# Performance work log

Measured on AMD Instinct MI355X. Metric: run time of the kernel, lower is better.

Reference implementation:

```python
import jax, jax.numpy as jnp
import numpy as np

BN_EPS = 1e-5


def setup_inputs() -> dict:
    key = jax.random.key(0)
    ks = jax.random.split(key, 8)
    N, Cin, Cout, D, H, W = 4, 512, 256, 256, 128, 128
    feat_ffm = jax.random.normal(ks[0], (N, Cin, H, W), dtype=jnp.float32)
    coarse_x = jax.random.normal(ks[1], (N, D, H, W), dtype=jnp.float32)
    # conv1: 1x1, no bias; BN (eval mode: running stats); conv2: 1x1 with bias
    w1 = jax.random.normal(ks[2], (Cout, Cin), dtype=jnp.float32) * (1.0 / np.sqrt(Cin))
    bn_gamma = jnp.ones((Cout,), dtype=jnp.float32)
    bn_beta = jnp.zeros((Cout,), dtype=jnp.float32)
    bn_mean = jax.random.normal(ks[3], (Cout,), dtype=jnp.float32) * 0.1
    bn_var = jax.random.uniform(ks[4], (Cout,), dtype=jnp.float32, minval=0.5, maxval=1.5)
    w2 = jax.random.normal(ks[5], (Cout, Cout), dtype=jnp.float32) * (1.0 / np.sqrt(Cout))
    b2 = jnp.zeros((Cout,), dtype=jnp.float32)
    return {"feat_ffm": feat_ffm, "coarse_x": coarse_x, "w1": w1,
            "bn_gamma": bn_gamma, "bn_beta": bn_beta, "bn_mean": bn_mean,
            "bn_var": bn_var, "w2": w2, "b2": b2}


def reference(feat_ffm, coarse_x, w1, bn_gamma, bn_beta, bn_mean, bn_var, w2, b2):
    N, D, H, W = coarse_x.shape
    # conv1 (1x1) + BN(eval) + ReLU; Dropout2d is identity in eval mode
    x = jnp.einsum('nihw,oi->nohw', feat_ffm, w1)
    scale = bn_gamma * jax.lax.rsqrt(bn_var + BN_EPS)
    x = x * scale[None, :, None, None] + (bn_beta - bn_mean * scale)[None, :, None, None]
    x = jax.nn.relu(x)  # [N, C, H, W]
    C = x.shape[1]
    q = coarse_x.reshape(N, D, H * W)          # proj_query / proj_value
    k = x.reshape(N, C, H * W)                 # proj_key (pre-permute)
    energy = jnp.einsum('nds,ncs->ndc', q, k)  # [N, D, C]
    energy_new = jnp.max(energy, axis=-1, keepdims=True) - energy
    attention = jax.nn.softmax(energy_new, axis=-1)        # [N, D, C]
    out = jnp.einsum('ndc,nds->ncs', attention, q)         # attention^T @ value
    out = out.reshape(N, C, H, W)
    out = jnp.einsum('nchw,oc->nohw', out, w2) + b2[None, :, None, None]
    return out
```

## Files before the change

kernel.cpp:

```cpp
#include <hip/hip_runtime.h>


#define S_DIM 16384
#define C_DIM 256
#define CIN 512

typedef unsigned short u16;
typedef _Float16 f16;
typedef __attribute__((ext_vector_type(8))) _Float16 f16x8;
typedef __attribute__((ext_vector_type(4))) float f32x4;

__device__ __forceinline__ u16 f2h(float x) {
    f16 h = (f16)x;
    return *(u16*)&h;
}
__device__ __forceinline__ float h2f(u16 u) {
    f16 h = *(f16*)&u;
    return (float)h;
}
__device__ __forceinline__ void gld16(const u16* g, u16* l) {
    __builtin_amdgcn_global_load_lds((const __attribute__((address_space(1))) void*)g,
                                     (__attribute__((address_space(3))) void*)l, 16, 0, 0);
}
__device__ __forceinline__ void gld16f(const float* g, float* l) {
    __builtin_amdgcn_global_load_lds((const __attribute__((address_space(1))) void*)g,
                                     (__attribute__((address_space(3))) void*)l, 16, 0, 0);
}

__global__ __launch_bounds__(256) void prep_kernel(
    const float* __restrict__ coarse, const float* __restrict__ w1,
    const float* __restrict__ gamma, const float* __restrict__ beta,
    const float* __restrict__ mean, const float* __restrict__ var,
    u16* __restrict__ qhi, u16* __restrict__ qlo,
    u16* __restrict__ w1hi, u16* __restrict__ w1lo, float* __restrict__ b1) {
    int b = blockIdx.x;
    int t = threadIdx.x;
    if (b < 4096) {
        size_t i = (size_t)b * 256 + t;
        for (size_t c = i; c < 4194304u; c += 1048576u) {
            float4 v = ((const float4*)coarse)[c];
            float vv[4] = {v.x, v.y, v.z, v.w};
            u16 h[4], l[4];
#pragma unroll
            for (int j = 0; j < 4; ++j) {
                h[j] = f2h(vv[j]);
                l[j] = f2h(vv[j] - h2f(h[j]));
            }
            *(uint2*)&qhi[c * 4] = *(uint2*)h;
            *(uint2*)&qlo[c * 4] = *(uint2*)l;
        }
    } else {
        int o = (b - 4096) * 16 + (t >> 4);
        int lane16 = t & 15;
        float sc = gamma[o] * rsqrtf(var[o] + 1e-5f);
        for (int i = lane16; i < CIN; i += 16) {
            float v = w1[o * CIN + i] * sc;
            u16 h = f2h(v);
            w1hi[o * CIN + i] = h;
            w1lo[o * CIN + i] = f2h(v - h2f(h));
        }
        if (lane16 == 0) b1[o] = beta[o] - mean[o] * sc;
    }
}

__global__ __launch_bounds__(256) void conv_kernel(
    const u16* __restrict__ w1hi, const u16* __restrict__ w1lo,
    const float* __restrict__ feat, const float* __restrict__ b1,
    u16* __restrict__ khi, u16* __restrict__ klo) {
    __shared__ u16 AhS[4096], AlS[4096];
    __shared__ float BfS[4096];
    int s0 = blockIdx.x * 128;
    int m0 = blockIdx.y * 128;
    int bz = blockIdx.z;
    int tid = threadIdx.x, wave = tid >> 6, lane = tid & 63;
    int quad = lane >> 4, l15 = lane & 15;
    int wm = wave >> 1, wn = wave & 1;

    int Lr = lane >> 2, Ls = lane & 3;
    int koff = (Ls ^ ((Lr >> 1) & 3)) * 8;
    const u16* gAh = w1hi + (size_t)(m0 + wave * 32 + Lr) * CIN + koff;
    const u16* gAl = w1lo + (size_t)(m0 + wave * 32 + Lr) * CIN + koff;
    u16* dAh = AhS + wave * 1024;
    u16* dAl = AlS + wave * 1024;

    int bcol = ((lane & 31) * 4) ^ ((wave & 1) << 4);
    const float* gB = feat + (size_t)bz * ((size_t)CIN * S_DIM)
                    + (size_t)(8 * wave + (lane >> 5)) * S_DIM + s0 + bcol;
    float* dB = BfS + wave * 1024;

    f32x4 zero = {0.f, 0.f, 0.f, 0.f};
    f32x4 acc[4][4];
#pragma unroll
    for (int i = 0; i < 4; ++i)
#pragma unroll
        for (int j = 0; j < 4; ++j) acc[i][j] = zero;

    for (int kb = 0; kb < CIN; kb += 32) {
        __syncthreads();
        gld16(gAh + kb, dAh);
        gld16(gAh + kb + 16 * CIN, dAh + 512);
        gld16(gAl + kb, dAl);
        gld16(gAl + kb + 16 * CIN, dAl + 512);
#pragma unroll
        for (int p = 0; p < 4; ++p)
            gld16f(gB + (size_t)(kb + 2 * p) * S_DIM, dB + p * 256);
        __syncthreads();

        f16x8 a_h[4], a_l[4];
        int axor = ((l15 >> 1) & 3);
        int ao = (wm * 64 + l15) * 32 + ((quad ^ axor) * 8);
#pragma unroll
        for (int t = 0; t < 4; ++t) {
            a_h[t] = *(const f16x8*)&AhS[ao + t * 512];
            a_l[t] = *(const f16x8*)&AlS[ao + t * 512];
        }
        f16x8 b_s[4];
        int fl = (quad & 1) << 4;
        const float* Brow = BfS + quad * 1024;
#pragma unroll
        for (int nt = 0; nt < 4; ++nt) {
            int nf = (wn * 64 + nt * 16 + l15) ^ fl;
            union { u16 u[8]; f16x8 v; } T;
#pragma unroll
            for (int j = 0; j < 8; ++j) T.u[j] = f2h(Brow[j * 128 + nf]);
            b_s[nt] = T.v;
        }
#pragma unroll
        for (int mt = 0; mt < 4; ++mt)
#pragma unroll
            for (int nt = 0; nt < 4; ++nt) {
                acc[mt][nt] = __builtin_amdgcn_mfma_f32_16x16x32_f16(a_h[mt], b_s[nt], acc[mt][nt], 0, 0, 0);
                acc[mt][nt] = __builtin_amdgcn_mfma_f32_16x16x32_f16(a_l[mt], b_s[nt], acc[mt][nt], 0, 0, 0);
            }
    }

#pragma unroll
    for (int mt = 0; mt < 4; ++mt) {
#pragma unroll
        for (int r = 0; r < 4; ++r) {
            int row = m0 + wm * 64 + mt * 16 + quad * 4 + r;
            float bi = b1[row];
#pragma unroll
            for (int nt = 0; nt < 4; ++nt) {
                int cc = s0 + wn * 64 + nt * 16 + l15;
                float v = fmaxf(acc[mt][nt][r] + bi, 0.f);
                u16 h = f2h(v);
                size_t o = (size_t)bz * 4194304 + (size_t)row * S_DIM + cc;
                khi[o] = h;
                klo[o] = f2h(v - h2f(h));
            }
        }
    }
}

__global__ __launch_bounds__(256) void energy_kernel(
    const u16* __restrict__ qhi, const u16* __restrict__ qlo,
    const u16* __restrict__ khi, const u16* __restrict__ klo,
    float* __restrict__ Ep) {
    __shared__ u16 AhS[4096], BhS[4096], AlS[4096], BlS[4096];
    int kBeg = blockIdx.x * 512;
    int m0 = (blockIdx.y >> 1) * 128;
    int n0 = (blockIdx.y & 1) * 128;
    int bz = blockIdx.z;
    int tid = threadIdx.x, wave = tid >> 6, lane = tid & 63;
    int quad = lane >> 4, l15 = lane & 15;
    int wm = wave >> 1, wn = wave & 1;

    int Lr = lane >> 2, Ls = lane & 3;
    int koff = (Ls ^ ((Lr >> 1) & 3)) * 8;
    size_t bo = (size_t)bz * 4194304;
    const u16* gAh = qhi + bo + (size_t)(m0 + wave * 32 + Lr) * S_DIM + kBeg + koff;
    const u16* gAl = qlo + bo + (size_t)(m0 + wave * 32 + Lr) * S_DIM + kBeg + koff;
    const u16* gBh = khi + bo + (size_t)(n0 + wave * 32 + Lr) * S_DIM + kBeg + koff;
    const u16* gBl = klo + bo + (size_t)(n0 + wave * 32 + Lr) * S_DIM + kBeg + koff;
    u16* dAh = AhS + wave * 1024;
    u16* dAl = AlS + wave * 1024;
    u16* dBh = BhS + wave * 1024;
    u16* dBl = BlS + wave * 1024;

    f32x4 zero = {0.f, 0.f, 0.f, 0.f};
    f32x4 acc[4][4];
#pragma unroll
    for (int i = 0; i < 4; ++i)
#pragma unroll
        for (int j = 0; j < 4; ++j) acc[i][j] = zero;

    const size_t row16 = (size_t)16 * S_DIM;
    for (int kb = 0; kb < 512; kb += 32) {
        __syncthreads();
        gld16(gAh + kb, dAh);
        gld16(gAh + kb + row16, dAh + 512);
        gld16(gBh + kb, dBh);
        gld16(gBh + kb + row16, dBh + 512);
        gld16(gAl + kb, dAl);
        gld16(gAl + kb + row16, dAl + 512);
        gld16(gBl + kb, dBl);
        gld16(gBl + kb + row16, dBl + 512);
        __syncthreads();

        f16x8 a_h[4], b_h[4], a_l[4], b_l[4];
        int axor = ((l15 >> 1) & 3);
        int aOff = (wm * 64 + l15) * 32 + ((quad ^ axor) * 8);
        int bOff = (wn * 64 + l15) * 32 + ((quad ^ axor) * 8);
#pragma unroll
        for (int t = 0; t < 4; ++t) {
            a_h[t] = *(const f16x8*)&AhS[aOff + t * 512];
            b_h[t] = *(const f16x8*)&BhS[bOff + t * 512];
            a_l[t] = *(const f16x8*)&AlS[aOff + t * 512];
            b_l[t] = *(const f16x8*)&BlS[bOff + t * 512];
        }
#pragma unroll
        for (int mt = 0; mt < 4; ++mt)
#pragma unroll
            for (int nt = 0; nt < 4; ++nt) {
                acc[mt][nt] = __builtin_amdgcn_mfma_f32_16x16x32_f16(a_h[mt], b_h[nt], acc[mt][nt], 0, 0, 0);
                acc[mt][nt] = __builtin_amdgcn_mfma_f32_16x16x32_f16(a_h[mt], b_l[nt], acc[mt][nt], 0, 0, 0);
                acc[mt][nt] = __builtin_amdgcn_mfma_f32_16x16x32_f16(a_l[mt], b_h[nt], acc[mt][nt], 0, 0, 0);
            }
    }

    float* Ce = Ep + ((size_t)(blockIdx.x * 4 + bz)) * 65536;
#pragma unroll
    for (int mt = 0; mt < 4; ++mt)
#pragma unroll
        for (int r = 0; r < 4; ++r) {
            int row = m0 + wm * 64 + mt * 16 + quad * 4 + r;
#pragma unroll
            for (int nt = 0; nt < 4; ++nt) {
                int cc = n0 + wn * 64 + nt * 16 + l15;
                Ce[(size_t)row * C_DIM + cc] = acc[mt][nt][r];
            }
        }
}

__global__ __launch_bounds__(256) void softmax_kernel(const float* __restrict__ Ep,
                                                      float* __restrict__ att) {
    __shared__ float red[4], red2[4];
    int b = blockIdx.x;
    int t = threadIdx.x;
    const float* p = Ep + (size_t)b * 256 + t;
    float v = 0.f;
#pragma unroll 8
    for (int s = 0; s < 32; ++s) v += p[(size_t)s * 262144];
    float m = v;
#pragma unroll
    for (int o = 32; o > 0; o >>= 1) m = fminf(m, __shfl_xor(m, o, 64));
    int lane = t & 63, wid = t >> 6;
    if (lane == 0) red[wid] = m;
    __syncthreads();
    m = fminf(fminf(red[0], red[1]), fminf(red[2], red[3]));
    float e = expf(m - v);
    float s = e;
#pragma unroll
    for (int o = 32; o > 0; o >>= 1) s += __shfl_xor(s, o, 64);
    if (lane == 0) red2[wid] = s;
    __syncthreads();
    s = red2[0] + red2[1] + red2[2] + red2[3];
    att[(size_t)b * 256 + t] = e / s;
}

__global__ __launch_bounds__(256) void m2h_kernel(const float* __restrict__ w2,
                                                  const float* __restrict__ att,
                                                  u16* __restrict__ M2h) {
    int t = blockIdx.x * 256 + threadIdx.x;
    int d = t & 255, o = (t >> 8) & 255, n = t >> 16;
    const float4* wr = (const float4*)(w2 + (size_t)o * C_DIM);
    const float4* ar = (const float4*)(att + ((size_t)n * C_DIM + d) * C_DIM);
    float s = 0.0f;
#pragma unroll 4
    for (int c4 = 0; c4 < 64; ++c4) {
        float4 w = wr[c4];
        float4 a = ar[c4];
        s += w.x * a.x + w.y * a.y + w.z * a.z + w.w * a.w;
    }
    M2h[((size_t)n * C_DIM + o) * C_DIM + d] = f2h(s);
}

__global__ __launch_bounds__(256) void final_kernel(
    const u16* __restrict__ M2h, const float* __restrict__ coarse,
    const float* __restrict__ b2, float* __restrict__ out) {
    __shared__ u16 AhS[4096];
    __shared__ float BfS[4096];
    int s0 = blockIdx.x * 128;
    int m0 = blockIdx.y * 128;
    int bz = blockIdx.z;
    int tid = threadIdx.x, wave = tid >> 6, lane = tid & 63;
    int quad = lane >> 4, l15 = lane & 15;
    int wm = wave >> 1, wn = wave & 1;

    int Lr = lane >> 2, Ls = lane & 3;
    int koff = (Ls ^ ((Lr >> 1) & 3)) * 8;
    const u16* gA = M2h + (size_t)bz * 65536 + (size_t)(m0 + wave * 32 + Lr) * C_DIM + koff;
    u16* dA = AhS + wave * 1024;
    int bcol = ((lane & 31) * 4) ^ ((wave & 1) << 4);
    const float* gB = coarse + (size_t)bz * 4194304
                    + (size_t)(8 * wave + (lane >> 5)) * S_DIM + s0 + bcol;
    float* dB = BfS + wave * 1024;

    f32x4 zero = {0.f, 0.f, 0.f, 0.f};
    f32x4 acc[4][4];
#pragma unroll
    for (int i = 0; i < 4; ++i)
#pragma unroll
        for (int j = 0; j < 4; ++j) acc[i][j] = zero;

    for (int kb = 0; kb < C_DIM; kb += 32) {
        __syncthreads();
        gld16(gA + kb, dA);
        gld16(gA + kb + 16 * C_DIM, dA + 512);
#pragma unroll
        for (int p = 0; p < 4; ++p)
            gld16f(gB + (size_t)(kb + 2 * p) * S_DIM, dB + p * 256);
        __syncthreads();

        f16x8 a_s[4];
        int axor = ((l15 >> 1) & 3);
        int ao = (wm * 64 + l15) * 32 + ((quad ^ axor) * 8);
#pragma unroll
        for (int t = 0; t < 4; ++t) a_s[t] = *(const f16x8*)&AhS[ao + t * 512];
        f16x8 b_s[4];
        int fl = (quad & 1) << 4;
        const float* Brow = BfS + quad * 1024;
#pragma unroll
        for (int nt = 0; nt < 4; ++nt) {
            int nf = (wn * 64 + nt * 16 + l15) ^ fl;
            union { u16 u[8]; f16x8 v; } T;
#pragma unroll
            for (int j = 0; j < 8; ++j) T.u[j] = f2h(Brow[j * 128 + nf]);
            b_s[nt] = T.v;
        }
#pragma unroll
        for (int mt = 0; mt < 4; ++mt)
#pragma unroll
            for (int nt = 0; nt < 4; ++nt)
                acc[mt][nt] = __builtin_amdgcn_mfma_f32_16x16x32_f16(a_s[mt], b_s[nt], acc[mt][nt], 0, 0, 0);
    }

#pragma unroll
    for (int mt = 0; mt < 4; ++mt)
#pragma unroll
        for (int r = 0; r < 4; ++r) {
            int row = m0 + wm * 64 + mt * 16 + quad * 4 + r;
            float bi = b2[row];
#pragma unroll
            for (int nt = 0; nt < 4; ++nt) {
                int cc = s0 + wn * 64 + nt * 16 + l15;
                out[(size_t)bz * 4194304 + (size_t)row * S_DIM + cc] = acc[mt][nt][r] + bi;
            }
        }
}

extern "C" void kernel_launch(void* const* d_in, const int* in_sizes, int n_in,
                              void* d_out, int out_size, void* d_ws, size_t ws_size,
                              hipStream_t stream) {
    const float* feat   = (const float*)d_in[0];
    const float* coarse = (const float*)d_in[1];
    const float* w1     = (const float*)d_in[2];
    const float* gamma  = (const float*)d_in[3];
    const float* beta   = (const float*)d_in[4];
    const float* mean   = (const float*)d_in[5];
    const float* var    = (const float*)d_in[6];
    const float* w2     = (const float*)d_in[7];
    const float* b2     = (const float*)d_in[8];
    float* out = (float*)d_out;

    char* base = (char*)d_ws;
    u16* qhi   = (u16*)(base);
    u16* qlo   = (u16*)(base + 33554432);
    u16* khi   = (u16*)(base + 67108864);
    u16* klo   = (u16*)(base + 100663296);
    float* Ep  = (float*)(base + 134217728);
    float* att = (float*)(base + 201326592);
    u16* M2h   = (u16*)(base + 202375168);
    u16* w1hi  = (u16*)(base + 202899456);
    u16* w1lo  = (u16*)(base + 203161600);
    float* b1  = (float*)(base + 203423744);

    prep_kernel<<<4112, 256, 0, stream>>>(coarse, w1, gamma, beta, mean, var,
                                          qhi, qlo, w1hi, w1lo, b1);

    conv_kernel<<<dim3(128, 2, 4), 256, 0, stream>>>(w1hi, w1lo, feat, b1, khi, klo);

    energy_kernel<<<dim3(32, 4, 4), 256, 0, stream>>>(qhi, qlo, khi, klo, Ep);

    softmax_kernel<<<1024, 256, 0, stream>>>(Ep, att);

    m2h_kernel<<<1024, 256, 0, stream>>>(w2, att, M2h);

    final_kernel<<<dim3(128, 2, 4), 256, 0, stream>>>(M2h, coarse, b2, out);
}
```

Measured before the change: 428.6 us.

## Double-buffer LDS tiles in conv, energy and final GEMM kernels

The conv, energy and final GEMM kernels now keep two LDS buffers per operand. Each iteration issues the async global-to-LDS loads for the next K tile before computing on the current one, leaving one barrier per iteration instead of two. The aim is to hide global load latency behind the MFMA work. In exchange, LDS use per block doubles, which can lower occupancy, and the compiler may still insert conservative waits that remove the overlap.

Result: no change. 423.1 us (-1.3%).

```diff
diff --git a/kernel.cpp b/kernel.cpp
--- a/kernel.cpp
+++ b/kernel.cpp
@@ -25,6 +25,17 @@
 __device__ __forceinline__ void gld16f(const float* g, float* l) {
     __builtin_amdgcn_global_load_lds((const __attribute__((address_space(1))) void*)g,
                                      (__attribute__((address_space(3))) void*)l, 16, 0, 0);
+}
+
+__device__ __forceinline__ void stage_pair(const u16* g, int kb, size_t row16,
+                                           u16* d, int wave) {
+    gld16(g + kb, d + wave * 1024);
+    gld16(g + kb + row16, d + wave * 1024 + 512);
+}
+__device__ __forceinline__ void stage_b(const float* g, int kb, float* d, int wave) {
+#pragma unroll
+    for (int p = 0; p < 4; ++p)
+        gld16f(g + (size_t)(kb + 2 * p) * S_DIM, d + wave * 1024 + p * 256);
 }
 
 __global__ __launch_bounds__(256) void prep_kernel(
@@ -67,8 +78,8 @@
     const u16* __restrict__ w1hi, const u16* __restrict__ w1lo,
     const float* __restrict__ feat, const float* __restrict__ b1,
     u16* __restrict__ khi, u16* __restrict__ klo) {
-    __shared__ u16 AhS[4096], AlS[4096];
-    __shared__ float BfS[4096];
+    __shared__ u16 AhS[2][4096], AlS[2][4096];
+    __shared__ float BfS[2][4096];
     int s0 = blockIdx.x * 128;
     int m0 = blockIdx.y * 128;
     int bz = blockIdx.z;
@@ -80,13 +91,9 @@
     int koff = (Ls ^ ((Lr >> 1) & 3)) * 8;
     const u16* gAh = w1hi + (size_t)(m0 + wave * 32 + Lr) * CIN + koff;
     const u16* gAl = w1lo + (size_t)(m0 + wave * 32 + Lr) * CIN + koff;
-    u16* dAh = AhS + wave * 1024;
-    u16* dAl = AlS + wave * 1024;
-
     int bcol = ((lane & 31) * 4) ^ ((wave & 1) << 4);
     const float* gB = feat + (size_t)bz * ((size_t)CIN * S_DIM)
                     + (size_t)(8 * wave + (lane >> 5)) * S_DIM + s0 + bcol;
-    float* dB = BfS + wave * 1024;
 
     f32x4 zero = {0.f, 0.f, 0.f, 0.f};
     f32x4 acc[4][4];
@@ -95,28 +102,30 @@
 #pragma unroll
         for (int j = 0; j < 4; ++j) acc[i][j] = zero;
 
+    stage_pair(gAh, 0, 16 * CIN, AhS[0], wave);
+    stage_pair(gAl, 0, 16 * CIN, AlS[0], wave);
+    stage_b(gB, 0, BfS[0], wave);
+    __syncthreads();
+
+    int cur = 0;
     for (int kb = 0; kb < CIN; kb += 32) {
-        __syncthreads();
-        gld16(gAh + kb, dAh);
-        gld16(gAh + kb + 16 * CIN, dAh + 512);
-        gld16(gAl + kb, dAl);
-        gld16(gAl + kb + 16 * CIN, dAl + 512);
-#pragma unroll
-        for (int p = 0; p < 4; ++p)
-            gld16f(gB + (size_t)(kb + 2 * p) * S_DIM, dB + p * 256);
-        __syncthreads();
+        if (kb + 32 < CIN) {
+            stage_pair(gAh, kb + 32, 16 * CIN, AhS[cur ^ 1], wave);
+            stage_pair(gAl, kb + 32, 16 * CIN, AlS[cur ^ 1], wave);
+            stage_b(gB, kb + 32, BfS[cur ^ 1], wave);
+        }
 
         f16x8 a_h[4], a_l[4];
         int axor = ((l15 >> 1) & 3);
         int ao = (wm * 64 + l15) * 32 + ((quad ^ axor) * 8);
 #pragma unroll
         for (int t = 0; t < 4; ++t) {
-            a_h[t] = *(const f16x8*)&AhS[ao + t * 512];
-            a_l[t] = *(const f16x8*)&AlS[ao + t * 512];
+            a_h[t] = *(const f16x8*)&AhS[cur][ao + t * 512];
+            a_l[t] = *(const f16x8*)&AlS[cur][ao + t * 512];
         }
         f16x8 b_s[4];
         int fl = (quad & 1) << 4;
-        const float* Brow = BfS + quad * 1024;
+        const float* Brow = BfS[cur] + quad * 1024;
 #pragma unroll
         for (int nt = 0; nt < 4; ++nt) {
             int nf = (wn * 64 + nt * 16 + l15) ^ fl;
@@ -132,6 +141,8 @@
                 acc[mt][nt] = __builtin_amdgcn_mfma_f32_16x16x32_f16(a_h[mt], b_s[nt], acc[mt][nt], 0, 0, 0);
                 acc[mt][nt] = __builtin_amdgcn_mfma_f32_16x16x32_f16(a_l[mt], b_s[nt], acc[mt][nt], 0, 0, 0);
             }
+        __syncthreads();
+        cur ^= 1;
     }
 
 #pragma unroll
@@ -157,7 +168,7 @@
     const u16* __restrict__ qhi, const u16* __restrict__ qlo,
     const u16* __restrict__ khi, const u16* __restrict__ klo,
     float* __restrict__ Ep) {
-    __shared__ u16 AhS[4096], BhS[4096], AlS[4096], BlS[4096];
+    __shared__ u16 AhS[2][4096], BhS[2][4096], AlS[2][4096], BlS[2][4096];
     int kBeg = blockIdx.x * 512;
     int m0 = (blockIdx.y >> 1) * 128;
     int n0 = (blockIdx.y & 1) * 128;
@@ -173,10 +184,6 @@
     const u16* gAl = qlo + bo + (size_t)(m0 + wave * 32 + Lr) * S_DIM + kBeg + koff;
     const u16* gBh = khi + bo + (size_t)(n0 + wave * 32 + Lr) * S_DIM + kBeg + koff;
     const u16* gBl = klo + bo + (size_t)(n0 + wave * 32 + Lr) * S_DIM + kBeg + koff;
-    u16* dAh = AhS + wave * 1024;
-    u16* dAl = AlS + wave * 1024;
-    u16* dBh = BhS + wave * 1024;
-    u16* dBl = BlS + wave * 1024;
 
     f32x4 zero = {0.f, 0.f, 0.f, 0.f};
     f32x4 acc[4][4];
@@ -186,17 +193,20 @@
         for (int j = 0; j < 4; ++j) acc[i][j] = zero;
 
     const size_t row16 = (size_t)16 * S_DIM;
+    stage_pair(gAh, 0, row16, AhS[0], wave);
+    stage_pair(gBh, 0, row16, BhS[0], wave);
+    stage_pair(gAl, 0, row16, AlS[0], wave);
+    stage_pair(gBl, 0, row16, BlS[0], wave);
+    __syncthreads();
+
+    int cur = 0;
     for (int kb = 0; kb < 512; kb += 32) {
-        __syncthreads();
-        gld16(gAh + kb, dAh);
-        gld16(gAh + kb + row16, dAh + 512);
-        gld16(gBh + kb, dBh);
-        gld16(gBh + kb + row16, dBh + 512);
-        gld16(gAl + kb, dAl);
-        gld16(gAl + kb + row16, dAl + 512);
-        gld16(gBl + kb, dBl);
-        gld16(gBl + kb + row16, dBl + 512);
-        __syncthreads();
+        if (kb + 32 < 512) {
+            stage_pair(gAh, kb + 32, row16, AhS[cur ^ 1], wave);
+            stage_pair(gBh, kb + 32, row16, BhS[cur ^ 1], wave);
+            stage_pair(gAl, kb + 32, row16, AlS[cur ^ 1], wave);
+            stage_pair(gBl, kb + 32, row16, BlS[cur ^ 1], wave);
+        }
 
         f16x8 a_h[4], b_h[4], a_l[4], b_l[4];
         int axor = ((l15 >> 1) & 3);
@@ -204,10 +214,10 @@
         int bOff = (wn * 64 + l15) * 32 + ((quad ^ axor) * 8);
 #pragma unroll
         for (int t = 0; t < 4; ++t) {
-            a_h[t] = *(const f16x8*)&AhS[aOff + t * 512];
-            b_h[t] = *(const f16x8*)&BhS[bOff + t * 512];
-            a_l[t] = *(const f16x8*)&AlS[aOff + t * 512];
-            b_l[t] = *(const f16x8*)&BlS[bOff + t * 512];
+            a_h[t] = *(const f16x8*)&AhS[cur][aOff + t * 512];
+            b_h[t] = *(const f16x8*)&BhS[cur][bOff + t * 512];
+            a_l[t] = *(const f16x8*)&AlS[cur][aOff + t * 512];
+            b_l[t] = *(const f16x8*)&BlS[cur][bOff + t * 512];
         }
 #pragma unroll
         for (int mt = 0; mt < 4; ++mt)
@@ -217,6 +227,8 @@
                 acc[mt][nt] = __builtin_amdgcn_mfma_f32_16x16x32_f16(a_h[mt], b_l[nt], acc[mt][nt], 0, 0, 0);
                 acc[mt][nt] = __builtin_amdgcn_mfma_f32_16x16x32_f16(a_l[mt], b_h[nt], acc[mt][nt], 0, 0, 0);
             }
+        __syncthreads();
+        cur ^= 1;
     }
 
     float* Ce = Ep + ((size_t)(blockIdx.x * 4 + bz)) * 65536;
@@ -279,8 +291,8 @@
 __global__ __launch_bounds__(256) void final_kernel(
     const u16* __restrict__ M2h, const float* __restrict__ coarse,
     const float* __restrict__ b2, float* __restrict__ out) {
-    __shared__ u16 AhS[4096];
-    __shared__ float BfS[4096];
+    __shared__ u16 AhS[2][4096];
+    __shared__ float BfS[2][4096];
     int s0 = blockIdx.x * 128;
     int m0 = blockIdx.y * 128;
     int bz = blockIdx.z;
@@ -291,11 +303,9 @@
     int Lr = lane >> 2, Ls = lane & 3;
     int koff = (Ls ^ ((Lr >> 1) & 3)) * 8;
     const u16* gA = M2h + (size_t)bz * 65536 + (size_t)(m0 + wave * 32 + Lr) * C_DIM + koff;
-    u16* dA = AhS + wave * 1024;
     int bcol = ((lane & 31) * 4) ^ ((wave & 1) << 4);
     const float* gB = coarse + (size_t)bz * 4194304
                     + (size_t)(8 * wave + (lane >> 5)) * S_DIM + s0 + bcol;
-    float* dB = BfS + wave * 1024;
 
     f32x4 zero = {0.f, 0.f, 0.f, 0.f};
     f32x4 acc[4][4];
@@ -304,23 +314,25 @@
 #pragma unroll
         for (int j = 0; j < 4; ++j) acc[i][j] = zero;
 
+    stage_pair(gA, 0, 16 * C_DIM, AhS[0], wave);
+    stage_b(gB, 0, BfS[0], wave);
+    __syncthreads();
+
+    int cur = 0;
     for (int kb = 0; kb < C_DIM; kb += 32) {
-        __syncthreads();
-        gld16(gA + kb, dA);
-        gld16(gA + kb + 16 * C_DIM, dA + 512);
-#pragma unroll
-        for (int p = 0; p < 4; ++p)
-            gld16f(gB + (size_t)(kb + 2 * p) * S_DIM, dB + p * 256);
-        __syncthreads();
+        if (kb + 32 < C_DIM) {
+            stage_pair(gA, kb + 32, 16 * C_DIM, AhS[cur ^ 1], wave);
+            stage_b(gB, kb + 32, BfS[cur ^ 1], wave);
+        }
 
         f16x8 a_s[4];
         int axor = ((l15 >> 1) & 3);
         int ao = (wm * 64 + l15) * 32 + ((quad ^ axor) * 8);
 #pragma unroll
-        for (int t = 0; t < 4; ++t) a_s[t] = *(const f16x8*)&AhS[ao + t * 512];
+        for (int t = 0; t < 4; ++t) a_s[t] = *(const f16x8*)&AhS[cur][ao + t * 512];
         f16x8 b_s[4];
         int fl = (quad & 1) << 4;
-        const float* Brow = BfS + quad * 1024;
+        const float* Brow = BfS[cur] + quad * 1024;
 #pragma unroll
         for (int nt = 0; nt < 4; ++nt) {
             int nf = (wn * 64 + nt * 16 + l15) ^ fl;
@@ -334,6 +346,8 @@
 #pragma unroll
             for (int nt = 0; nt < 4; ++nt)
                 acc[mt][nt] = __builtin_amdgcn_mfma_f32_16x16x32_f16(a_s[mt], b_s[nt], acc[mt][nt], 0, 0, 0);
+        __syncthreads();
+        cur ^= 1;
     }
 
 #pragma unroll
```
